# Optimization experiments

Hardware: AMD Instinct MI355X
Metric: run time of the kernel (lower is better)

## Reference

```python
import jax, jax.numpy as jnp
import numpy as np

HEADS = 12
EMBED = 768
HEAD_DIM = EMBED // HEADS


def setup_inputs() -> dict:
    key = jax.random.key(0)
    kx, kw, kb = jax.random.split(key, 3)
    x = jax.random.normal(kx, (8, 1024, EMBED), dtype=jnp.float32)
    # nn.Linear(embed, 3*embed): weight (3E, E), bias (3E,)
    W_qkv = jax.random.normal(kw, (3 * EMBED, EMBED), dtype=jnp.float32) * (1.0 / np.sqrt(EMBED))
    b_qkv = jax.random.normal(kb, (3 * EMBED,), dtype=jnp.float32) * 0.01
    return {"x": x, "W_qkv": W_qkv, "b_qkv": b_qkv}


def reference(x, W_qkv, b_qkv):
    b, n, e = x.shape
    qkv = x @ W_qkv.T + b_qkv                       # (b, n, 3E)
    qkv = qkv.reshape(b, n, HEADS, 3 * HEAD_DIM)    # (b, n, h, 3d)
    q, k, v = jnp.split(qkv, 3, axis=-1)            # each (b, n, h, d)
    scores = jnp.einsum('bihd,bjhd->bijh', q, k) / np.sqrt(HEAD_DIM)
    attn = jax.nn.softmax(scores, axis=-2)          # softmax over keys j (dim=-2)
    out = jnp.einsum('bijh,bjhd->bihd', attn, v)
    return out.reshape(b, n, e)
```

## Files before the change

### kernel.cpp

```cpp
#include <hip/hip_runtime.h>
#include <hip/hip_bf16.h>
#include <cstdint>
#include <math.h>

#define BATCH 8
#define SEQ   1024
#define EMB   768
#define HEADS 12
#define HDIM  64
#define C3    2304
#define MROWS (BATCH*SEQ)
#define NKT   (EMB / 32)
#define MTILES (MROWS / 128)
#define NTILES (C3 / 128)
#define XPACK_BLOCKS (MTILES * NKT)
#define WPACK_BLOCKS (NTILES * NKT)

typedef __attribute__((ext_vector_type(8)))  short bf16x8;
typedef __attribute__((ext_vector_type(4)))  short bf16x4;
typedef __attribute__((ext_vector_type(4)))  float f32x4;

static __device__ inline short f2bf(float f) {
    union { float f; uint32_t u; } v; v.f = f;
    uint32_t u = v.u + 0x7fff + ((v.u >> 16) & 1);
    return (short)(u >> 16);
}

static __device__ __forceinline__ void gload_lds16(const short* g, short* l) {
    __builtin_amdgcn_global_load_lds(
        (const __attribute__((address_space(1))) unsigned int*)g,
        (__attribute__((address_space(3))) unsigned int*)l, 16, 0, 0);
}

__global__ __launch_bounds__(256) void pack_bf16(const float* __restrict__ x,
                                                 short* __restrict__ xb2,
                                                 const float* __restrict__ W,
                                                 short* __restrict__ Wb2) {
    const float* in;
    short* out;
    int blk;
    if (blockIdx.x < XPACK_BLOCKS) {
        in = x; out = xb2; blk = blockIdx.x;
    } else {
        in = W; out = Wb2; blk = blockIdx.x - XPACK_BLOCKS;
    }
    const int mt = blk / NKT;
    const int kt = blk % NKT;
    short* obase = out + (size_t)blk * 4096;

    #pragma unroll
    for (int p = 0; p < 2; ++p) {
        int idx = p * 256 + threadIdx.x;
        int r = idx >> 2, s = idx & 3;
        const float* src = in + (size_t)(mt * 128 + r) * EMB + kt * 32 + s * 8;
        float4 v0 = ((const float4*)src)[0];
        float4 v1 = ((const float4*)src)[1];
        bf16x8 o = { f2bf(v0.x), f2bf(v0.y), f2bf(v0.z), f2bf(v0.w),
                     f2bf(v1.x), f2bf(v1.y), f2bf(v1.z), f2bf(v1.w) };
        int S = ((4 * r + s) ^ (r & 7));
        *(bf16x8*)(obase + S * 8) = o;
    }
}

__global__ __launch_bounds__(256) void qkv_gemm_mfma(const short* __restrict__ Apk,
                                                     const short* __restrict__ Bpk,
                                                     const float* __restrict__ bias,
                                                     short* __restrict__ qkvb) {
    __shared__ short As[2][4096];
    __shared__ short Bs[2][4096];

    const int g    = blockIdx.x;
    const int xcd  = g & 7;
    const int ring = g >> 3;
    const int by   = xcd * 8 + (ring & 7);
    const int bx   = ring >> 3;

    const int t    = threadIdx.x;
    const int w    = t >> 6;
    const int lane = t & 63;
    const int s4   = lane >> 4;
    const int r15  = lane & 15;
    const int m0 = by * 128, n0 = bx * 128;
    const int wm = (w & 1) * 64, wn = (w >> 1) * 64;

    const short* Ab = Apk + (size_t)by * (NKT * 4096);
    const short* Bb = Bpk + (size_t)bx * (NKT * 4096);

    int offA[4], offB[4];
    #pragma unroll
    for (int i = 0; i < 4; ++i) {
        int ra = wm + i * 16 + r15;
        offA[i] = ((4 * ra + s4) ^ (ra & 7)) << 3;
        int rb = wn + i * 16 + r15;
        offB[i] = ((4 * rb + s4) ^ (rb & 7)) << 3;
    }

    const int seg0 = w * 2;

#define STAGE(buf, kt) do {                                                   \
        const short* _a = Ab + (size_t)(kt) * 4096;                           \
        const short* _b = Bb + (size_t)(kt) * 4096;                           \
        gload_lds16(_a + (seg0    ) * 512 + lane * 8, &As[buf][(seg0    ) * 512]); \
        gload_lds16(_b + (seg0    ) * 512 + lane * 8, &Bs[buf][(seg0    ) * 512]); \
        gload_lds16(_a + (seg0 + 1) * 512 + lane * 8, &As[buf][(seg0 + 1) * 512]); \
        gload_lds16(_b + (seg0 + 1) * 512 + lane * 8, &Bs[buf][(seg0 + 1) * 512]); \
    } while (0)

    f32x4 acc[4][4] = {};

#define COMPUTE(buf) do {                                                     \
        bf16x8 af[4], bff[4];                                                 \
        _Pragma("unroll")                                                     \
        for (int i = 0; i < 4; ++i) {                                         \
            af[i]  = *(const bf16x8*)&As[buf][offA[i]];                       \
            bff[i] = *(const bf16x8*)&Bs[buf][offB[i]];                       \
        }                                                                     \
        _Pragma("unroll")                                                     \
        for (int mi = 0; mi < 4; ++mi)                                        \
            _Pragma("unroll")                                                 \
            for (int ni = 0; ni < 4; ++ni)                                    \
                acc[mi][ni] = __builtin_amdgcn_mfma_f32_16x16x32_bf16(        \
                    af[mi], bff[ni], acc[mi][ni], 0, 0, 0);                   \
    } while (0)

    STAGE(0, 0);
    __syncthreads();

    for (int kt = 0; kt < NKT; kt += 2) {
        STAGE(1, kt + 1);
        COMPUTE(0);
        __syncthreads();
        if (kt + 2 < NKT) STAGE(0, kt + 2);
        COMPUTE(1);
        __syncthreads();
    }
#undef STAGE
#undef COMPUTE

    float bsv[4], scl[4];
    #pragma unroll
    for (int ni = 0; ni < 4; ++ni) {
        int n = n0 + wn + ni * 16 + r15;
        bsv[ni] = bias[n];
        scl[ni] = ((n % 192) < 64) ? 0.125f : 1.0f;
    }
    #pragma unroll
    for (int mi = 0; mi < 4; ++mi)
        #pragma unroll
        for (int ni = 0; ni < 4; ++ni) {
            int n = n0 + wn + ni * 16 + r15;
            #pragma unroll
            for (int reg = 0; reg < 4; ++reg) {
                int m = m0 + wm + mi * 16 + s4 * 4 + reg;
                qkvb[(size_t)m * C3 + n] = f2bf((acc[mi][ni][reg] + bsv[ni]) * scl[ni]);
            }
        }
}

__global__ __launch_bounds__(256) void v_transpose(const short* __restrict__ qkvb,
                                                   short* __restrict__ vt) {
    __shared__ int Lt[64][65];

    const int bh = blockIdx.x;
    const int jt = blockIdx.y;
    const int b = bh / HEADS, h = bh % HEADS;
    const int t = threadIdx.x;
    const int j0 = jt * 64;
    const size_t base = (size_t)b * SEQ * C3 + (size_t)h * 192 + 128;

    #pragma unroll
    for (int p = 0; p < 2; ++p) {
        int idx = p * 256 + t;
        int j = idx >> 3, d0 = (idx & 7) * 8;
        bf16x8 v = *(const bf16x8*)(qkvb + base + (size_t)(j0 + j) * C3 + d0);
        #pragma unroll
        for (int u = 0; u < 8; ++u)
            Lt[d0 + u][j] = (int)(unsigned short)v[u];
    }
    __syncthreads();
    #pragma unroll
    for (int p = 0; p < 2; ++p) {
        int idx = p * 256 + t;
        int d = idx >> 3, c8 = (idx & 7) * 8;
        bf16x8 o;
        #pragma unroll
        for (int u = 0; u < 8; ++u)
            o[u] = (short)Lt[d][c8 + u];
        *(bf16x8*)(vt + ((size_t)bh * 64 + d) * SEQ + j0 + c8) = o;
    }
}

__global__ __launch_bounds__(256, 4) void attn_mfma(const short* __restrict__ qkvb,
                                                    const short* __restrict__ vt,
                                                    float* __restrict__ out) {
    __shared__ short Ks[64][64];
    __shared__ short Vt[64][64];
    __shared__ short Ps[64][64];

    const int g    = blockIdx.x;
    const int qt   = g / (BATCH * HEADS);
    const int bh   = g % (BATCH * HEADS);
    const int b    = bh / HEADS;
    const int h    = bh % HEADS;
    const int t    = threadIdx.x;
    const int w    = t >> 6;
    const int lane = t & 63;
    const int c    = lane & 15;
    const int q    = lane >> 4;
    const int ck   = c & 7;
    const int i0   = qt * 64;

    const size_t base = (size_t)b * SEQ * C3 + (size_t)h * 192;
    const short* vtb = vt + (size_t)bh * 64 * SEQ;
    const short* gk  = qkvb + base + 64;

    bf16x8 aq0, aq1;
    {
        const short* pq = qkvb + base + (size_t)(i0 + w * 16 + c) * C3 + q * 8;
        aq0 = *(const bf16x8*)(pq);
        aq1 = *(const bf16x8*)(pq + 32);
    }

    const int jA = t >> 3;
    const int jB = jA + 32;
    const int sg = t & 7;
    const int wKA = (sg ^ (jA & 7)) * 8;
    const int wKB = (sg ^ (jB & 7)) * 8;

    bf16x8 kr0, kr1, vr0, vr1;
    kr0 = *(const bf16x8*)(gk + (size_t)jA * C3 + sg * 8);
    kr1 = *(const bf16x8*)(gk + (size_t)jB * C3 + sg * 8);
    vr0 = *(const bf16x8*)(vtb + (size_t)jA * SEQ + sg * 8);
    vr1 = *(const bf16x8*)(vtb + (size_t)jB * SEQ + sg * 8);

    f32x4 o[4] = {};
    float l_acc = 0.f;

    for (int kt = 0; kt < 16; ++kt) {
        __syncthreads();
        *(bf16x8*)&Ks[jA][wKA] = kr0;
        *(bf16x8*)&Ks[jB][wKB] = kr1;
        *(bf16x8*)&Vt[jA][wKA] = vr0;
        *(bf16x8*)&Vt[jB][wKB] = vr1;
        __syncthreads();

        if (kt < 15) {
            const int j0 = (kt + 1) * 64;
            kr0 = *(const bf16x8*)(gk + (size_t)(j0 + jA) * C3 + sg * 8);
            kr1 = *(const bf16x8*)(gk + (size_t)(j0 + jB) * C3 + sg * 8);
            vr0 = *(const bf16x8*)(vtb + (size_t)jA * SEQ + j0 + sg * 8);
            vr1 = *(const bf16x8*)(vtb + (size_t)jB * SEQ + j0 + sg * 8);
        }

        bf16x8 ka[4][2];
        #pragma unroll
        for (int mt = 0; mt < 4; ++mt) {
            ka[mt][0] = *(bf16x8*)&Ks[mt * 16 + c][(q ^ ck) * 8];
            ka[mt][1] = *(bf16x8*)&Ks[mt * 16 + c][((4 + q) ^ ck) * 8];
        }

        f32x4 s[4];
        __builtin_amdgcn_s_setprio(1);
        #pragma unroll
        for (int mt = 0; mt < 4; ++mt) {
            f32x4 acc = {0.f, 0.f, 0.f, 0.f};
            acc = __builtin_amdgcn_mfma_f32_16x16x32_bf16(ka[mt][0], aq0, acc, 0, 0, 0);
            acc = __builtin_amdgcn_mfma_f32_16x16x32_bf16(ka[mt][1], aq1, acc, 0, 0, 0);
            s[mt] = acc;
        }
        __builtin_amdgcn_s_setprio(0);

        #pragma unroll
        for (int mt = 0; mt < 4; ++mt) {
            float p0 = __expf(s[mt][0]);
            float p1 = __expf(s[mt][1]);
            float p2 = __expf(s[mt][2]);
            float p3 = __expf(s[mt][3]);
            l_acc += (p0 + p1) + (p2 + p3);
            bf16x4 pw = { f2bf(p0), f2bf(p1), f2bf(p2), f2bf(p3) };
            int pcol = (((2 * mt + (q >> 1)) ^ ck) << 3) + (q & 1) * 4;
            *(bf16x4*)&Ps[w * 16 + c][pcol] = pw;
        }

        bf16x8 vb[4][2];
        #pragma unroll
        for (int dt = 0; dt < 4; ++dt) {
            vb[dt][0] = *(bf16x8*)&Vt[dt * 16 + c][(q ^ ck) * 8];
            vb[dt][1] = *(bf16x8*)&Vt[dt * 16 + c][((4 + q) ^ ck) * 8];
        }

        bf16x8 ap0 = *(bf16x8*)&Ps[w * 16 + c][(q ^ ck) * 8];
        bf16x8 ap1 = *(bf16x8*)&Ps[w * 16 + c][((4 + q) ^ ck) * 8];
        __builtin_amdgcn_s_setprio(1);
        #pragma unroll
        for (int dt = 0; dt < 4; ++dt) {
            o[dt] = __builtin_amdgcn_mfma_f32_16x16x32_bf16(ap0, vb[dt][0], o[dt], 0, 0, 0);
            o[dt] = __builtin_amdgcn_mfma_f32_16x16x32_bf16(ap1, vb[dt][1], o[dt], 0, 0, 0);
        }
        __builtin_amdgcn_s_setprio(0);
    }

    float v = l_acc;
    v += __shfl_xor(v, 16, 64);
    v += __shfl_xor(v, 32, 64);
    float linv[4];
    #pragma unroll
    for (int r = 0; r < 4; ++r)
        linv[r] = 1.0f / __shfl(v, 4 * q + r, 64);

    #pragma unroll
    for (int dt = 0; dt < 4; ++dt)
        #pragma unroll
        for (int r = 0; r < 4; ++r) {
            int i = w * 16 + q * 4 + r;
            out[((size_t)b * SEQ + i0 + i) * EMB + h * HDIM + dt * 16 + c]
                = o[dt][r] * linv[r];
        }
}

extern "C" void kernel_launch(void* const* d_in, const int* in_sizes, int n_in,
                              void* d_out, int out_size, void* d_ws, size_t ws_size,
                              hipStream_t stream) {
    const float* x    = (const float*)d_in[0];
    const float* W    = (const float*)d_in[1];
    const float* bias = (const float*)d_in[2];
    float* out = (float*)d_out;

    short* xb2  = (short*)d_ws;
    short* Wb2  = xb2 + (size_t)MROWS * EMB;
    short* qkvb = Wb2 + (size_t)C3 * EMB;
    short* vt   = qkvb + (size_t)MROWS * C3;

    pack_bf16<<<XPACK_BLOCKS + WPACK_BLOCKS, 256, 0, stream>>>(x, xb2, W, Wb2);

    qkv_gemm_mfma<<<1152, 256, 0, stream>>>(xb2, Wb2, bias, qkvb);

    dim3 g2(BATCH * HEADS, SEQ / 64);
    v_transpose<<<g2, 256, 0, stream>>>(qkvb, vt);

    attn_mfma<<<BATCH * HEADS * (SEQ / 64), 256, 0, stream>>>(qkvb, vt, out);
}
```

Measured before the change: 169.2 us.

## Fuse V transpose into QKV GEMM epilogue via shared-memory staging

The separate v_transpose kernel is removed. Waves of the QKV GEMM that hold V columns now write their bias-added bf16 tile into a padded shared-memory buffer, which reuses the GEMM's As/Bs space, and then store it transposed straight into the vt layout. This drops one kernel launch and one full read and write of V through global memory. In exchange the epilogue gains an extra block barrier and branching between V and non-V waves. The V columns are also no longer written to qkvb.

```diff
diff --git a/kernel.cpp b/kernel.cpp
--- a/kernel.cpp
+++ b/kernel.cpp
@@ -62,12 +62,17 @@
     }
 }
 
+#define LVP 136
+
 __global__ __launch_bounds__(256) void qkv_gemm_mfma(const short* __restrict__ Apk,
                                                      const short* __restrict__ Bpk,
                                                      const float* __restrict__ bias,
-                                                     short* __restrict__ qkvb) {
-    __shared__ short As[2][4096];
-    __shared__ short Bs[2][4096];
+                                                     short* __restrict__ qkvb,
+                                                     short* __restrict__ vt) {
+    __shared__ short smem[16384];
+    short (*As)[4096] = (short (*)[4096])smem;
+    short (*Bs)[4096] = (short (*)[4096])(smem + 8192);
+    short* Lv = smem;
 
     const int g    = blockIdx.x;
     const int xcd  = g & 7;
@@ -137,6 +142,11 @@
 #undef STAGE
 #undef COMPUTE
 
+    const int bxm   = bx % 3;
+    const bool has_v    = (bxm != 0);
+    const int  wn_v     = (bxm == 1) ? 0 : 64;
+    const bool is_vwave = has_v && (wn == wn_v);
+
     float bsv[4], scl[4];
     #pragma unroll
     for (int ni = 0; ni < 4; ++ni) {
@@ -144,49 +154,50 @@
         bsv[ni] = bias[n];
         scl[ni] = ((n % 192) < 64) ? 0.125f : 1.0f;
     }
-    #pragma unroll
-    for (int mi = 0; mi < 4; ++mi)
-        #pragma unroll
-        for (int ni = 0; ni < 4; ++ni) {
-            int n = n0 + wn + ni * 16 + r15;
+
+    if (!is_vwave) {
+        #pragma unroll
+        for (int mi = 0; mi < 4; ++mi) {
+            const int m = m0 + wm + mi * 16 + s4 * 4;
             #pragma unroll
-            for (int reg = 0; reg < 4; ++reg) {
-                int m = m0 + wm + mi * 16 + s4 * 4 + reg;
-                qkvb[(size_t)m * C3 + n] = f2bf((acc[mi][ni][reg] + bsv[ni]) * scl[ni]);
+            for (int ni = 0; ni < 4; ++ni) {
+                const int n = n0 + wn + ni * 16 + r15;
+                #pragma unroll
+                for (int reg = 0; reg < 4; ++reg)
+                    qkvb[(size_t)(m + reg) * C3 + n] =
+                        f2bf((acc[mi][ni][reg] + bsv[ni]) * scl[ni]);
             }
         }
-}
-
-__global__ __launch_bounds__(256) void v_transpose(const short* __restrict__ qkvb,
-                                                   short* __restrict__ vt) {
-    __shared__ int Lt[64][65];
-
-    const int bh = blockIdx.x;
-    const int jt = blockIdx.y;
-    const int b = bh / HEADS, h = bh % HEADS;
-    const int t = threadIdx.x;
-    const int j0 = jt * 64;
-    const size_t base = (size_t)b * SEQ * C3 + (size_t)h * 192 + 128;
-
-    #pragma unroll
-    for (int p = 0; p < 2; ++p) {
-        int idx = p * 256 + t;
-        int j = idx >> 3, d0 = (idx & 7) * 8;
-        bf16x8 v = *(const bf16x8*)(qkvb + base + (size_t)(j0 + j) * C3 + d0);
-        #pragma unroll
-        for (int u = 0; u < 8; ++u)
-            Lt[d0 + u][j] = (int)(unsigned short)v[u];
-    }
-    __syncthreads();
-    #pragma unroll
-    for (int p = 0; p < 2; ++p) {
-        int idx = p * 256 + t;
-        int d = idx >> 3, c8 = (idx & 7) * 8;
-        bf16x8 o;
-        #pragma unroll
-        for (int u = 0; u < 8; ++u)
-            o[u] = (short)Lt[d][c8 + u];
-        *(bf16x8*)(vt + ((size_t)bh * 64 + d) * SEQ + j0 + c8) = o;
+    } else {
+        #pragma unroll
+        for (int mi = 0; mi < 4; ++mi) {
+            const int jl = wm + mi * 16 + s4 * 4;
+            #pragma unroll
+            for (int ni = 0; ni < 4; ++ni) {
+                const int d = ni * 16 + r15;
+                bf16x4 vv = { f2bf(acc[mi][ni][0] + bsv[ni]),
+                              f2bf(acc[mi][ni][1] + bsv[ni]),
+                              f2bf(acc[mi][ni][2] + bsv[ni]),
+                              f2bf(acc[mi][ni][3] + bsv[ni]) };
+                *(bf16x4*)&Lv[d * LVP + jl] = vv;
+            }
+        }
+    }
+
+    if (has_v) {
+        __syncthreads();
+        const int h  = (n0 + wn_v) / 192;
+        const int bb = by >> 3;
+        const int j0 = m0 & 1023;
+        short* vrow = vt + ((size_t)(bb * HEADS + h) * 64) * SEQ + j0;
+        #pragma unroll
+        for (int p = 0; p < 4; ++p) {
+            int lin = p * 256 + t;
+            int d   = lin >> 4;
+            int ch  = lin & 15;
+            *(bf16x8*)(vrow + (size_t)d * SEQ + ch * 8) =
+                *(bf16x8*)&Lv[d * LVP + ch * 8];
+        }
     }
 }
 
@@ -333,10 +344,7 @@
 
     pack_bf16<<<XPACK_BLOCKS + WPACK_BLOCKS, 256, 0, stream>>>(x, xb2, W, Wb2);
 
-    qkv_gemm_mfma<<<1152, 256, 0, stream>>>(xb2, Wb2, bias, qkvb);
-
-    dim3 g2(BATCH * HEADS, SEQ / 64);
-    v_transpose<<<g2, 256, 0, stream>>>(qkvb, vt);
+    qkv_gemm_mfma<<<1152, 256, 0, stream>>>(xb2, Wb2, bias, qkvb, vt);
 
     attn_mfma<<<BATCH * HEADS * (SEQ / 64), 256, 0, stream>>>(qkvb, vt, out);
 }
```

Result: no change. 172.1 us (+1.7%).
